# Kernel optimization log

Measured on AMD Instinct MI355X. Metric: run time of the kernel, lower is better.

The kernel has to match this reference:

```python
import jax, jax.numpy as jnp
from jax import lax
import numpy as np

# pywt sym4 analysis filters (pywt.Wavelet('sym4').dec_lo / .dec_hi)
DEC_LO = np.array([-0.07576571478927333, -0.02963552764599851, 0.49761866763201545,
                   0.8037387518059161, 0.29785779560527736, -0.09921954357684722,
                   -0.012603967262037833, 0.0322231006040427], dtype=np.float32)
DEC_HI = np.array([-0.0322231006040427, -0.012603967262037833, 0.09921954357684722,
                   0.29785779560527736, -0.8037387518059161, 0.49761866763201545,
                   0.02963552764599851, -0.07576571478927333], dtype=np.float32)
L = 8            # sym4 filter length
LEVEL = 4
THRESH = 10.0


def _conv1d(x, kernel, stride, pad):
    # x: (B, T), kernel: (L,) used in correlation sense by lax.conv
    y = lax.conv_general_dilated(x[:, None, :], kernel[None, None, :],
                                 window_strides=(stride,), padding=[pad],
                                 dimension_numbers=('NCH', 'OIH', 'NCH'))
    return y[:, 0, :]


def _dwt1(x, filt):
    # pywt single-level DWT, mode='symmetric':
    #   pad L-1 each side (half-sample symmetric), true convolution, take odd-index
    #   outputs of the 'valid' part -> length floor((N+L-1)/2)
    ext = jnp.pad(x, ((0, 0), (L - 1, L - 1)), mode='symmetric')[:, 1:]
    return _conv1d(ext, filt[::-1], 2, (0, 0))  # flip -> true convolution


def _idwt1(cA, cD, lo, hi):
    # pywt single-level IDWT: upsample by 2, full-convolve with rec filters, sum,
    # trim L-2 from the left, output length 2*n - L + 2.
    B, n = cA.shape
    upA = jnp.zeros((B, 2 * n), cA.dtype).at[:, ::2].set(cA)
    upD = jnp.zeros((B, 2 * n), cD.dtype).at[:, ::2].set(cD)
    # rec_lo = dec_lo[::-1]; full conv w/ rec_lo == correlation w/ dec_lo
    y = _conv1d(upA, lo, 1, (L - 1, L - 1)) + _conv1d(upD, hi, 1, (L - 1, L - 1))
    return y[:, L - 2: L - 2 + 2 * n - L + 2]


def _wavelet_denoise(x):
    lo = jnp.asarray(DEC_LO)
    hi = jnp.asarray(DEC_HI)
    a = x
    details = []
    for _ in range(LEVEL):
        details.append(_dwt1(a, hi))
        a = _dwt1(a, lo)
    # hard threshold: KEEP coefficients with |c| <= threshold, zero the rest
    details = [jnp.where(jnp.abs(d) <= THRESH, d, jnp.zeros_like(d)) for d in details]
    rec = a
    for d in reversed(details):
        if rec.shape[1] > d.shape[1]:     # pywt waverec a[:-1] trim
            rec = rec[:, :d.shape[1]]
        rec = _idwt1(rec, d, lo, hi)
    return rec


def setup_inputs() -> dict:
    key = jax.random.key(0)
    k1, k2 = jax.random.split(key)
    x = jax.random.normal(k1, (100000, 512), dtype=jnp.float32) * 20.0
    edge_index = jax.random.randint(k2, (2, 100000), 0, 100000, dtype=jnp.int64)
    return {"x": x, "edge_index": edge_index, "num_nodes": 100000}


def reference(x, edge_index, num_nodes):
    # edge_index / num_nodes are unused by the original forward
    return _wavelet_denoise(x)
```

## Files before the change

kernel.cpp:

```cpp
#include <hip/hip_runtime.h>
#include <cstddef>

typedef float f2 __attribute__((ext_vector_type(2)));
typedef float f4 __attribute__((ext_vector_type(4)));
typedef _Float16 h2 __attribute__((ext_vector_type(2)));
typedef _Float16 h8 __attribute__((ext_vector_type(8)));

#define THRESH_V 10.0f
#define WPB 2
#define SLICE_F2 930

static __device__ __forceinline__ void wave_sync() {
  asm volatile("s_waitcnt lgkmcnt(0)" ::: "memory");
}

#define L0f (-0.07576571478927333f)
#define L1f (-0.02963552764599851f)
#define L2f ( 0.49761866763201545f)
#define L3f ( 0.8037387518059161f)
#define L4f ( 0.29785779560527736f)
#define L5f (-0.09921954357684722f)
#define L6f (-0.012603967262037833f)
#define L7f ( 0.0322231006040427f)
#define H0f (-0.0322231006040427f)
#define H1f (-0.012603967262037833f)
#define H2f ( 0.09921954357684722f)
#define H3f ( 0.29785779560527736f)
#define H4f (-0.8037387518059161f)
#define H5f ( 0.49761866763201545f)
#define H6f ( 0.02963552764599851f)
#define H7f (-0.07576571478927333f)

static __device__ __forceinline__ f2 lo2(f4 w) { return __builtin_shufflevector(w, w, 0, 1); }
static __device__ __forceinline__ f2 hi2(f4 w) { return __builtin_shufflevector(w, w, 2, 3); }
static __device__ __forceinline__ float thr(float x) {
  return (fabsf(x) <= THRESH_V) ? x : 0.f;
}

template <int N, int B, bool MARGINS, bool D16>
static __device__ __forceinline__ void fwd_stage(const f2* __restrict__ in,
                                                 f2* __restrict__ ca,
                                                 void* __restrict__ cdv, int lane) {
#pragma clang fp contract(off)
  constexpr int M = (N + 7) >> 1;
  f2* const cdf = (f2*)cdv;
  h2* const cdh = (h2*)cdv;
  const int i0 = B * lane;
  if (i0 < M) {
    f2 w[2 * B + 6];
    const f4* p = (const f4*)(in + 2 * i0 - 6);
#pragma unroll
    for (int k = 0; k < B + 3; ++k) {
      const f4 t = p[k];
      w[2 * k] = lo2(t);
      w[2 * k + 1] = hi2(t);
    }
    f2 sA[B], sD[B];
#pragma unroll
    for (int j = 0; j < B; ++j) {
      const f2 v0 = w[2*j+0], v1 = w[2*j+1], v2 = w[2*j+2], v3 = w[2*j+3];
      const f2 v4 = w[2*j+4], v5 = w[2*j+5], v6 = w[2*j+6], v7 = w[2*j+7];
      f2 sLo = ((v0 * L7f + v1 * L6f) + (v2 * L5f + v3 * L4f)) +
               ((v4 * L3f + v5 * L2f) + (v6 * L1f + v7 * L0f));
      f2 sHi = ((v0 * H7f + v1 * H6f) + (v2 * H5f + v3 * H4f)) +
               ((v4 * H3f + v5 * H2f) + (v6 * H1f + v7 * H0f));
      sA[j] = sLo;
      f2 d; d.x = thr(sHi.x); d.y = thr(sHi.y);
      sD[j] = d;
      if constexpr (MARGINS) {
        const int i = i0 + j;
        if (i < 6)                 ca[-1 - i]        = sLo;
        if (i >= M - 7 && i < M)   ca[2 * M - 1 - i] = sLo;
      }
    }
    if (i0 + B <= M) {
      if constexpr (B == 4) {
        f4 c0; c0.x=sA[0].x; c0.y=sA[0].y; c0.z=sA[1].x; c0.w=sA[1].y;
        f4 c1; c1.x=sA[2].x; c1.y=sA[2].y; c1.z=sA[3].x; c1.w=sA[3].y;
        *(f4*)(ca + i0)     = c0;
        *(f4*)(ca + i0 + 2) = c1;
        if constexpr (D16) {
          h8 hv;
          hv[0]=(_Float16)sD[0].x; hv[1]=(_Float16)sD[0].y;
          hv[2]=(_Float16)sD[1].x; hv[3]=(_Float16)sD[1].y;
          hv[4]=(_Float16)sD[2].x; hv[5]=(_Float16)sD[2].y;
          hv[6]=(_Float16)sD[3].x; hv[7]=(_Float16)sD[3].y;
          *(h8*)(cdh + i0) = hv;
        } else {
          f4 d0; d0.x=sD[0].x; d0.y=sD[0].y; d0.z=sD[1].x; d0.w=sD[1].y;
          f4 d1; d1.x=sD[2].x; d1.y=sD[2].y; d1.z=sD[3].x; d1.w=sD[3].y;
          *(f4*)(cdf + i0)     = d0;
          *(f4*)(cdf + i0 + 2) = d1;
        }
      } else if constexpr (B == 2) {
        f4 c0; c0.x=sA[0].x; c0.y=sA[0].y; c0.z=sA[1].x; c0.w=sA[1].y;
        *(f4*)(ca + i0) = c0;
        if constexpr (D16) {
          h2 r0; r0.x=(_Float16)sD[0].x; r0.y=(_Float16)sD[0].y;
          h2 r1; r1.x=(_Float16)sD[1].x; r1.y=(_Float16)sD[1].y;
          cdh[i0] = r0; cdh[i0 + 1] = r1;
        } else {
          f4 d0; d0.x=sD[0].x; d0.y=sD[0].y; d0.z=sD[1].x; d0.w=sD[1].y;
          *(f4*)(cdf + i0) = d0;
        }
      } else {
#pragma unroll
        for (int j = 0; j < B; ++j) {
          ca[i0 + j] = sA[j];
          if constexpr (D16) {
            h2 r; r.x=(_Float16)sD[j].x; r.y=(_Float16)sD[j].y;
            cdh[i0 + j] = r;
          } else cdf[i0 + j] = sD[j];
        }
      }
    } else {
#pragma unroll
      for (int j = 0; j < B; ++j) {
        const int i = i0 + j;
        if (i < M) {
          ca[i] = sA[j];
          if constexpr (D16) {
            h2 r; r.x=(_Float16)sD[j].x; r.y=(_Float16)sD[j].y;
            cdh[i] = r;
          } else cdf[i] = sD[j];
        }
      }
    }
  }
  if constexpr (64 * B < M) {
    const int it = 64 * B + lane;
    if (it < M) {
      f2 w2[8];
      const f4* p2 = (const f4*)(in + 2 * it - 6);
#pragma unroll
      for (int k = 0; k < 4; ++k) { const f4 t = p2[k]; w2[2*k]=lo2(t); w2[2*k+1]=hi2(t); }
      const f2 v0=w2[0],v1=w2[1],v2=w2[2],v3=w2[3],v4=w2[4],v5=w2[5],v6=w2[6],v7=w2[7];
      f2 sLo = ((v0 * L7f + v1 * L6f) + (v2 * L5f + v3 * L4f)) +
               ((v4 * L3f + v5 * L2f) + (v6 * L1f + v7 * L0f));
      f2 sHi = ((v0 * H7f + v1 * H6f) + (v2 * H5f + v3 * H4f)) +
               ((v4 * H3f + v5 * H2f) + (v6 * H1f + v7 * H0f));
      ca[it] = sLo;
      if constexpr (MARGINS) {
        if (it >= M - 7) ca[2 * M - 1 - it] = sLo;
      }
      f2 d; d.x = thr(sHi.x); d.y = thr(sHi.y);
      if constexpr (D16) {
        h2 r; r.x=(_Float16)d.x; r.y=(_Float16)d.y;
        cdh[it] = r;
      } else cdf[it] = d;
    }
  }
}

template <int OUT, int B, bool D16, bool GOUT>
static __device__ __forceinline__ void inv_stage(const f2* __restrict__ ca,
                                                 const void* __restrict__ cdv,
                                                 f2* __restrict__ dst,
                                                 float* __restrict__ gA,
                                                 float* __restrict__ gB,
                                                 bool hasB, int lane) {
#pragma clang fp contract(fast)
  constexpr int P = (OUT + 1) >> 1;
  const f2* const cf = (const f2*)cdv;
  const h2* const ch = (const h2*)cdv;
  const int t0 = B * lane;
  if (t0 < P) {
    f2 a[B + 3], e[B + 3];
    if constexpr (B == 1) {
#pragma unroll
      for (int k = 0; k < 4; ++k) {
        a[k] = ca[t0 + k];
        if constexpr (D16) { const h2 hx = ch[t0+k]; e[k].x=(float)hx.x; e[k].y=(float)hx.y; }
        else e[k] = cf[t0 + k];
      }
    } else {
      constexpr int NR = (B + 4) / 2;
      const f4* pa = (const f4*)(ca + t0);
#pragma unroll
      for (int k = 0; k < NR; ++k) {
        const f4 t = pa[k];
        if (2 * k     < B + 3) a[2 * k]     = lo2(t);
        if (2 * k + 1 < B + 3) a[2 * k + 1] = hi2(t);
      }
      if constexpr (D16) {
        const f4* ph = (const f4*)(ch + t0);
        const f4 r0 = ph[0], r1 = ph[1];
        const float rr[8] = {r0.x, r0.y, r0.z, r0.w, r1.x, r1.y, r1.z, r1.w};
#pragma unroll
        for (int k = 0; k < B + 3; ++k) {
          const h2 hx = __builtin_bit_cast(h2, rr[k]);
          e[k].x = (float)hx.x; e[k].y = (float)hx.y;
        }
      } else {
        const f4* pe = (const f4*)(cf + t0);
#pragma unroll
        for (int k = 0; k < NR; ++k) {
          const f4 t = pe[k];
          if (2 * k     < B + 3) e[2 * k]     = lo2(t);
          if (2 * k + 1 < B + 3) e[2 * k + 1] = hi2(t);
        }
      }
    }
    f2 SE[B], SO[B];
#pragma unroll
    for (int j = 0; j < B; ++j) {
      const f2 a0=a[j], a1=a[j+1], a2=a[j+2], a3=a[j+3];
      const f2 e0=e[j], e1=e[j+1], e2=e[j+2], e3=e[j+3];
      SE[j] = a0*L1f + a1*L3f + a2*L5f + a3*L7f +
              e0*H1f + e1*H3f + e2*H5f + e3*H7f;
      SO[j] = a0*L0f + a1*L2f + a2*L4f + a3*L6f +
              e0*H0f + e1*H2f + e2*H4f + e3*H6f;
    }
    if constexpr (GOUT) {
      const int q0 = 2 * t0;
      *reinterpret_cast<float4*>(gA + q0)     = make_float4(SE[0].x, SO[0].x, SE[1].x, SO[1].x);
      *reinterpret_cast<float4*>(gA + q0 + 4) = make_float4(SE[2].x, SO[2].x, SE[3].x, SO[3].x);
      if (hasB) {
        *reinterpret_cast<float4*>(gB + q0)     = make_float4(SE[0].y, SO[0].y, SE[1].y, SO[1].y);
        *reinterpret_cast<float4*>(gB + q0 + 4) = make_float4(SE[2].y, SO[2].y, SE[3].y, SO[3].y);
      }
    } else {
      const bool full = (t0 + B <= P) && (2 * (t0 + B) <= OUT);
      if (full) {
#pragma unroll
        for (int j = 0; j < B; ++j) {
          f4 r; r.x=SE[j].x; r.y=SE[j].y; r.z=SO[j].x; r.w=SO[j].y;
          *(f4*)(dst + 2 * (t0 + j)) = r;
        }
      } else {
#pragma unroll
        for (int j = 0; j < B; ++j) {
          const int t = t0 + j;
          if (t < P) {
            const int q = 2 * t;
            dst[q] = SE[j];
            if (q + 1 < OUT) dst[q + 1] = SO[j];
          }
        }
      }
    }
  }
  if constexpr (64 * B < P) {
    const int tt = 64 * B + lane;
    if (tt < P) {
      const f2 a0=ca[tt], a1=ca[tt+1], a2=ca[tt+2], a3=ca[tt+3];
      f2 e0, e1, e2, e3;
      if constexpr (D16) {
        const h2 x0=ch[tt], x1=ch[tt+1], x2=ch[tt+2], x3=ch[tt+3];
        e0.x=(float)x0.x; e0.y=(float)x0.y; e1.x=(float)x1.x; e1.y=(float)x1.y;
        e2.x=(float)x2.x; e2.y=(float)x2.y; e3.x=(float)x3.x; e3.y=(float)x3.y;
      } else { e0=cf[tt]; e1=cf[tt+1]; e2=cf[tt+2]; e3=cf[tt+3]; }
      const f2 se = a0*L1f + a1*L3f + a2*L5f + a3*L7f +
                    e0*H1f + e1*H3f + e2*H5f + e3*H7f;
      const f2 so = a0*L0f + a1*L2f + a2*L4f + a3*L6f +
                    e0*H0f + e1*H2f + e2*H4f + e3*H6f;
      const int q = 2 * tt;
      dst[q] = se;
      if (q + 1 < OUT) dst[q + 1] = so;
    }
  }
}

__global__ __launch_bounds__(128, 5) void wavelet_denoise_kernel(
    const float* __restrict__ x, float* __restrict__ out, int nrows) {
  __shared__ __align__(16) f2 lds[WPB][SLICE_F2];
  const int wave = threadIdx.x >> 6;
  const int lane = threadIdx.x & 63;
  const int nPairs = (nrows + 1) >> 1;
  const int pairId = blockIdx.x * WPB + wave;
  if (pairId >= nPairs) return;

  const int rA = 2 * pairId;
  const bool hasB = (rA + 1) < nrows;
  const int rBc = hasB ? rA + 1 : rA;

  f2* Sp  = lds[wave];
  f2* sx  = Sp + 6;
  f2* ca2 = Sp + 6;    f2* d2 = Sp + 146;
  f2* ca3 = Sp + 286;  f2* d3 = Sp + 364;
  f2* ca4 = Sp + 436;  f2* d4 = Sp + 474;
  f2* rec133 = Sp + 0;
  f2* ca1 = Sp + 530;
  f2* rec70  = Sp + 524;
  f2* rec259 = Sp + 524;
  h2* d1  = (h2*)(Sp + 800);

  {
    const float4* sA4 = reinterpret_cast<const float4*>(x + (size_t)rA * 512);
    const float4* sB4 = reinterpret_cast<const float4*>(x + (size_t)rBc * 512);
#pragma unroll
    for (int kk = 0; kk < 2; ++kk) {
      const int c = lane + kk * 64;
      const float4 a = sA4[c];
      const float4 b = sB4[c];
      f4 u0; u0.x = a.x; u0.y = b.x; u0.z = a.y; u0.w = b.y;
      f4 u1; u1.x = a.z; u1.y = b.z; u1.z = a.w; u1.w = b.w;
      *reinterpret_cast<f4*>(sx + 4 * c)     = u0;
      *reinterpret_cast<f4*>(sx + 4 * c + 2) = u1;
      if (c == 0) {
        f4 m0; m0.x = a.y; m0.y = b.y; m0.z = a.x; m0.w = b.x;
        *reinterpret_cast<f4*>(sx - 2) = m0;
        f4 m1; m1.x = a.w; m1.y = b.w; m1.z = a.z; m1.w = b.z;
        *reinterpret_cast<f4*>(sx - 4) = m1;
      }
      if (c == 1) {
        f4 m; m.x = a.y; m.y = b.y; m.z = a.x; m.w = b.x;
        *reinterpret_cast<f4*>(sx - 6) = m;
      }
      if (c == 127) {
        f4 m0; m0.x = a.w; m0.y = b.w; m0.z = a.z; m0.w = b.z;
        *reinterpret_cast<f4*>(sx + 512) = m0;
        f4 m1; m1.x = a.y; m1.y = b.y; m1.z = a.x; m1.w = b.x;
        *reinterpret_cast<f4*>(sx + 514) = m1;
      }
      if (c == 126) {
        f4 m0; m0.x = a.w; m0.y = b.w; m0.z = a.z; m0.w = b.z;
        *reinterpret_cast<f4*>(sx + 516) = m0;
      }
    }
  }
  wave_sync();

  fwd_stage<512, 4, true,  true >(sx,  ca1, d1, lane); wave_sync();
  fwd_stage<259, 3, true,  false>(ca1, ca2, d2, lane); wave_sync();
  fwd_stage<133, 2, true,  false>(ca2, ca3, d3, lane); wave_sync();
  fwd_stage< 70, 1, false, false>(ca3, ca4, d4, lane); wave_sync();

  float* gA = out + (size_t)rA * 512;
  float* gB = out + (size_t)rBc * 512;
  inv_stage< 70, 1, false, false>(ca4,    d4, rec70,  nullptr, nullptr, false, lane);
  wave_sync();
  inv_stage<133, 2, false, false>(rec70,  d3, rec133, nullptr, nullptr, false, lane);
  wave_sync();
  inv_stage<259, 2, false, false>(rec133, d2, rec259, nullptr, nullptr, false, lane);
  wave_sync();
  inv_stage<512, 4, true,  true >(rec259, d1, nullptr, gA, gB, hasB, lane);
}

extern "C" void kernel_launch(void* const* d_in, const int* in_sizes, int n_in,
                              void* d_out, int out_size, void* d_ws, size_t ws_size,
                              hipStream_t stream) {
  const float* x = (const float*)d_in[0];
  float* out = (float*)d_out;
  const int nrows = in_sizes[0] / 512;
  const int nPairs = (nrows + 1) >> 1;
  const int grid = (nPairs + WPB - 1) / WPB;
  wavelet_denoise_kernel<<<dim3(grid), dim3(WPB * 64), 0, stream>>>(x, out, nrows);
}
```

Baseline: 339.1 us.

## Compute first DWT level from global loads and XOR-swizzle LDS layout

The first forward level now reads its input windows straight from global memory into registers, with symmetric padding handled in registers for edge lanes. This drops the initial staging of the interleaved input rows into LDS and one LDS round trip. All LDS buffers are renumbered as offsets into one slice and accessed through an XOR swizzle, which is meant to cut bank conflicts on the strided f4 accesses. In exchange, neighbouring lanes load overlapping global windows, so each input element is fetched about twice, and the swizzle adds integer work to every LDS address.

```diff
diff --git a/kernel.cpp b/kernel.cpp
--- a/kernel.cpp
+++ b/kernel.cpp
@@ -8,10 +8,26 @@
 
 #define THRESH_V 10.0f
 #define WPB 2
-#define SLICE_F2 930
+#define SLICE_F2 928
+
+#define CA2B 6
+#define D2B  146
+#define CA3B 286
+#define D3B  364
+#define CA4B 434
+#define D4B  472
+#define REC133B 0
+#define REC70B  510
+#define REC259B 510
+#define CA1B 516
+#define D1B  784
 
 static __device__ __forceinline__ void wave_sync() {
   asm volatile("s_waitcnt lgkmcnt(0)" ::: "memory");
+}
+
+static __device__ __forceinline__ int swz(int U) {
+  return U ^ (((U >> 4) & 7) << 1);
 }
 
 #define L0f (-0.07576571478927333f)
@@ -37,154 +53,91 @@
   return (fabsf(x) <= THRESH_V) ? x : 0.f;
 }
 
-template <int N, int B, bool MARGINS, bool D16>
-static __device__ __forceinline__ void fwd_stage(const f2* __restrict__ in,
-                                                 f2* __restrict__ ca,
-                                                 void* __restrict__ cdv, int lane) {
+static __device__ __forceinline__ void fwd_core(f2 v0, f2 v1, f2 v2, f2 v3,
+                                                f2 v4, f2 v5, f2 v6, f2 v7,
+                                                f2& sLo, f2& sHi) {
 #pragma clang fp contract(off)
+  sLo = ((v0 * L7f + v1 * L6f) + (v2 * L5f + v3 * L4f)) +
+        ((v4 * L3f + v5 * L2f) + (v6 * L1f + v7 * L0f));
+  sHi = ((v0 * H7f + v1 * H6f) + (v2 * H5f + v3 * H4f)) +
+        ((v4 * H3f + v5 * H2f) + (v6 * H1f + v7 * H0f));
+}
+
+template <int N, int B, bool MARGINS>
+static __device__ __forceinline__ void fwd_lds(f2* __restrict__ Sp, int INB,
+                                               int CAB, int DB, int lane) {
   constexpr int M = (N + 7) >> 1;
-  f2* const cdf = (f2*)cdv;
-  h2* const cdh = (h2*)cdv;
   const int i0 = B * lane;
   if (i0 < M) {
-    f2 w[2 * B + 6];
-    const f4* p = (const f4*)(in + 2 * i0 - 6);
+    f2 w[2 * (B + 3)];
+    const int u0 = INB + 2 * i0 - 6;
 #pragma unroll
     for (int k = 0; k < B + 3; ++k) {
-      const f4 t = p[k];
+      const f4 t = *(const f4*)(Sp + swz(u0 + 2 * k));
       w[2 * k] = lo2(t);
       w[2 * k + 1] = hi2(t);
     }
     f2 sA[B], sD[B];
 #pragma unroll
     for (int j = 0; j < B; ++j) {
-      const f2 v0 = w[2*j+0], v1 = w[2*j+1], v2 = w[2*j+2], v3 = w[2*j+3];
-      const f2 v4 = w[2*j+4], v5 = w[2*j+5], v6 = w[2*j+6], v7 = w[2*j+7];
-      f2 sLo = ((v0 * L7f + v1 * L6f) + (v2 * L5f + v3 * L4f)) +
-               ((v4 * L3f + v5 * L2f) + (v6 * L1f + v7 * L0f));
-      f2 sHi = ((v0 * H7f + v1 * H6f) + (v2 * H5f + v3 * H4f)) +
-               ((v4 * H3f + v5 * H2f) + (v6 * H1f + v7 * H0f));
-      sA[j] = sLo;
-      f2 d; d.x = thr(sHi.x); d.y = thr(sHi.y);
+      f2 lo, hi;
+      fwd_core(w[2*j+0], w[2*j+1], w[2*j+2], w[2*j+3],
+               w[2*j+4], w[2*j+5], w[2*j+6], w[2*j+7], lo, hi);
+      sA[j] = lo;
+      f2 d; d.x = thr(hi.x); d.y = thr(hi.y);
       sD[j] = d;
       if constexpr (MARGINS) {
         const int i = i0 + j;
-        if (i < 6)                 ca[-1 - i]        = sLo;
-        if (i >= M - 7 && i < M)   ca[2 * M - 1 - i] = sLo;
-      }
-    }
-    if (i0 + B <= M) {
-      if constexpr (B == 4) {
-        f4 c0; c0.x=sA[0].x; c0.y=sA[0].y; c0.z=sA[1].x; c0.w=sA[1].y;
-        f4 c1; c1.x=sA[2].x; c1.y=sA[2].y; c1.z=sA[3].x; c1.w=sA[3].y;
-        *(f4*)(ca + i0)     = c0;
-        *(f4*)(ca + i0 + 2) = c1;
-        if constexpr (D16) {
-          h8 hv;
-          hv[0]=(_Float16)sD[0].x; hv[1]=(_Float16)sD[0].y;
-          hv[2]=(_Float16)sD[1].x; hv[3]=(_Float16)sD[1].y;
-          hv[4]=(_Float16)sD[2].x; hv[5]=(_Float16)sD[2].y;
-          hv[6]=(_Float16)sD[3].x; hv[7]=(_Float16)sD[3].y;
-          *(h8*)(cdh + i0) = hv;
-        } else {
-          f4 d0; d0.x=sD[0].x; d0.y=sD[0].y; d0.z=sD[1].x; d0.w=sD[1].y;
-          f4 d1; d1.x=sD[2].x; d1.y=sD[2].y; d1.z=sD[3].x; d1.w=sD[3].y;
-          *(f4*)(cdf + i0)     = d0;
-          *(f4*)(cdf + i0 + 2) = d1;
-        }
-      } else if constexpr (B == 2) {
-        f4 c0; c0.x=sA[0].x; c0.y=sA[0].y; c0.z=sA[1].x; c0.w=sA[1].y;
-        *(f4*)(ca + i0) = c0;
-        if constexpr (D16) {
-          h2 r0; r0.x=(_Float16)sD[0].x; r0.y=(_Float16)sD[0].y;
-          h2 r1; r1.x=(_Float16)sD[1].x; r1.y=(_Float16)sD[1].y;
-          cdh[i0] = r0; cdh[i0 + 1] = r1;
-        } else {
-          f4 d0; d0.x=sD[0].x; d0.y=sD[0].y; d0.z=sD[1].x; d0.w=sD[1].y;
-          *(f4*)(cdf + i0) = d0;
-        }
-      } else {
-#pragma unroll
-        for (int j = 0; j < B; ++j) {
-          ca[i0 + j] = sA[j];
-          if constexpr (D16) {
-            h2 r; r.x=(_Float16)sD[j].x; r.y=(_Float16)sD[j].y;
-            cdh[i0 + j] = r;
-          } else cdf[i0 + j] = sD[j];
-        }
-      }
+        if (i < 6 && i < M)        Sp[swz(CAB - 1 - i)]         = lo;
+        if (i >= M - 7 && i < M)   Sp[swz(CAB + 2 * M - 1 - i)] = lo;
+      }
+    }
+    if constexpr (B == 2) {
+      f4 c; c.x = sA[0].x; c.y = sA[0].y; c.z = sA[1].x; c.w = sA[1].y;
+      *(f4*)(Sp + swz(CAB + i0)) = c;
+      f4 d; d.x = sD[0].x; d.y = sD[0].y; d.z = sD[1].x; d.w = sD[1].y;
+      *(f4*)(Sp + swz(DB + i0)) = d;
     } else {
 #pragma unroll
       for (int j = 0; j < B; ++j) {
         const int i = i0 + j;
         if (i < M) {
-          ca[i] = sA[j];
-          if constexpr (D16) {
-            h2 r; r.x=(_Float16)sD[j].x; r.y=(_Float16)sD[j].y;
-            cdh[i] = r;
-          } else cdf[i] = sD[j];
+          Sp[swz(CAB + i)] = sA[j];
+          Sp[swz(DB + i)]  = sD[j];
         }
       }
     }
   }
-  if constexpr (64 * B < M) {
-    const int it = 64 * B + lane;
-    if (it < M) {
-      f2 w2[8];
-      const f4* p2 = (const f4*)(in + 2 * it - 6);
-#pragma unroll
-      for (int k = 0; k < 4; ++k) { const f4 t = p2[k]; w2[2*k]=lo2(t); w2[2*k+1]=hi2(t); }
-      const f2 v0=w2[0],v1=w2[1],v2=w2[2],v3=w2[3],v4=w2[4],v5=w2[5],v6=w2[6],v7=w2[7];
-      f2 sLo = ((v0 * L7f + v1 * L6f) + (v2 * L5f + v3 * L4f)) +
-               ((v4 * L3f + v5 * L2f) + (v6 * L1f + v7 * L0f));
-      f2 sHi = ((v0 * H7f + v1 * H6f) + (v2 * H5f + v3 * H4f)) +
-               ((v4 * H3f + v5 * H2f) + (v6 * H1f + v7 * H0f));
-      ca[it] = sLo;
-      if constexpr (MARGINS) {
-        if (it >= M - 7) ca[2 * M - 1 - it] = sLo;
-      }
-      f2 d; d.x = thr(sHi.x); d.y = thr(sHi.y);
-      if constexpr (D16) {
-        h2 r; r.x=(_Float16)d.x; r.y=(_Float16)d.y;
-        cdh[it] = r;
-      } else cdf[it] = d;
-    }
-  }
 }
 
 template <int OUT, int B, bool D16, bool GOUT>
-static __device__ __forceinline__ void inv_stage(const f2* __restrict__ ca,
-                                                 const void* __restrict__ cdv,
-                                                 f2* __restrict__ dst,
-                                                 float* __restrict__ gA,
-                                                 float* __restrict__ gB,
-                                                 bool hasB, int lane) {
+static __device__ __forceinline__ void inv_lds(f2* __restrict__ Sp, int CAB,
+                                               int DB, int DSTB,
+                                               float* __restrict__ gA,
+                                               float* __restrict__ gB,
+                                               bool hasB, int lane) {
 #pragma clang fp contract(fast)
   constexpr int P = (OUT + 1) >> 1;
-  const f2* const cf = (const f2*)cdv;
-  const h2* const ch = (const h2*)cdv;
   const int t0 = B * lane;
   if (t0 < P) {
     f2 a[B + 3], e[B + 3];
     if constexpr (B == 1) {
 #pragma unroll
       for (int k = 0; k < 4; ++k) {
-        a[k] = ca[t0 + k];
-        if constexpr (D16) { const h2 hx = ch[t0+k]; e[k].x=(float)hx.x; e[k].y=(float)hx.y; }
-        else e[k] = cf[t0 + k];
+        a[k] = Sp[swz(CAB + t0 + k)];
+        e[k] = Sp[swz(DB + t0 + k)];
       }
     } else {
       constexpr int NR = (B + 4) / 2;
-      const f4* pa = (const f4*)(ca + t0);
 #pragma unroll
       for (int k = 0; k < NR; ++k) {
-        const f4 t = pa[k];
+        const f4 t = *(const f4*)(Sp + swz(CAB + t0 + 2 * k));
         if (2 * k     < B + 3) a[2 * k]     = lo2(t);
         if (2 * k + 1 < B + 3) a[2 * k + 1] = hi2(t);
       }
       if constexpr (D16) {
-        const f4* ph = (const f4*)(ch + t0);
-        const f4 r0 = ph[0], r1 = ph[1];
+        const f4 r0 = *(const f4*)(Sp + swz(DB + (t0 >> 1)));
+        const f4 r1 = *(const f4*)(Sp + swz(DB + (t0 >> 1) + 2));
         const float rr[8] = {r0.x, r0.y, r0.z, r0.w, r1.x, r1.y, r1.z, r1.w};
 #pragma unroll
         for (int k = 0; k < B + 3; ++k) {
@@ -192,10 +145,9 @@
           e[k].x = (float)hx.x; e[k].y = (float)hx.y;
         }
       } else {
-        const f4* pe = (const f4*)(cf + t0);
 #pragma unroll
         for (int k = 0; k < NR; ++k) {
-          const f4 t = pe[k];
+          const f4 t = *(const f4*)(Sp + swz(DB + t0 + 2 * k));
           if (2 * k     < B + 3) e[2 * k]     = lo2(t);
           if (2 * k + 1 < B + 3) e[2 * k + 1] = hi2(t);
         }
@@ -204,12 +156,10 @@
     f2 SE[B], SO[B];
 #pragma unroll
     for (int j = 0; j < B; ++j) {
-      const f2 a0=a[j], a1=a[j+1], a2=a[j+2], a3=a[j+3];
-      const f2 e0=e[j], e1=e[j+1], e2=e[j+2], e3=e[j+3];
-      SE[j] = a0*L1f + a1*L3f + a2*L5f + a3*L7f +
-              e0*H1f + e1*H3f + e2*H5f + e3*H7f;
-      SO[j] = a0*L0f + a1*L2f + a2*L4f + a3*L6f +
-              e0*H0f + e1*H2f + e2*H4f + e3*H6f;
+      SE[j] = a[j]*L1f + a[j+1]*L3f + a[j+2]*L5f + a[j+3]*L7f +
+              e[j]*H1f + e[j+1]*H3f + e[j+2]*H5f + e[j+3]*H7f;
+      SO[j] = a[j]*L0f + a[j+1]*L2f + a[j+2]*L4f + a[j+3]*L6f +
+              e[j]*H0f + e[j+1]*H2f + e[j+2]*H4f + e[j+3]*H6f;
     }
     if constexpr (GOUT) {
       const int q0 = 2 * t0;
@@ -224,8 +174,8 @@
       if (full) {
 #pragma unroll
         for (int j = 0; j < B; ++j) {
-          f4 r; r.x=SE[j].x; r.y=SE[j].y; r.z=SO[j].x; r.w=SO[j].y;
-          *(f4*)(dst + 2 * (t0 + j)) = r;
+          f4 r; r.x = SE[j].x; r.y = SE[j].y; r.z = SO[j].x; r.w = SO[j].y;
+          *(f4*)(Sp + swz(DSTB + 2 * (t0 + j))) = r;
         }
       } else {
 #pragma unroll
@@ -233,8 +183,8 @@
           const int t = t0 + j;
           if (t < P) {
             const int q = 2 * t;
-            dst[q] = SE[j];
-            if (q + 1 < OUT) dst[q + 1] = SO[j];
+            Sp[swz(DSTB + q)] = SE[j];
+            if (q + 1 < OUT) Sp[swz(DSTB + q + 1)] = SO[j];
           }
         }
       }
@@ -243,20 +193,17 @@
   if constexpr (64 * B < P) {
     const int tt = 64 * B + lane;
     if (tt < P) {
-      const f2 a0=ca[tt], a1=ca[tt+1], a2=ca[tt+2], a3=ca[tt+3];
-      f2 e0, e1, e2, e3;
-      if constexpr (D16) {
-        const h2 x0=ch[tt], x1=ch[tt+1], x2=ch[tt+2], x3=ch[tt+3];
-        e0.x=(float)x0.x; e0.y=(float)x0.y; e1.x=(float)x1.x; e1.y=(float)x1.y;
-        e2.x=(float)x2.x; e2.y=(float)x2.y; e3.x=(float)x3.x; e3.y=(float)x3.y;
-      } else { e0=cf[tt]; e1=cf[tt+1]; e2=cf[tt+2]; e3=cf[tt+3]; }
+      f2 a0 = Sp[swz(CAB + tt)],     a1 = Sp[swz(CAB + tt + 1)];
+      f2 a2 = Sp[swz(CAB + tt + 2)], a3 = Sp[swz(CAB + tt + 3)];
+      f2 e0 = Sp[swz(DB + tt)],      e1 = Sp[swz(DB + tt + 1)];
+      f2 e2 = Sp[swz(DB + tt + 2)],  e3 = Sp[swz(DB + tt + 3)];
       const f2 se = a0*L1f + a1*L3f + a2*L5f + a3*L7f +
                     e0*H1f + e1*H3f + e2*H5f + e3*H7f;
       const f2 so = a0*L0f + a1*L2f + a2*L4f + a3*L6f +
                     e0*H0f + e1*H2f + e2*H4f + e3*H6f;
       const int q = 2 * tt;
-      dst[q] = se;
-      if (q + 1 < OUT) dst[q + 1] = so;
+      Sp[swz(DSTB + q)] = se;
+      if (q + 1 < OUT) Sp[swz(DSTB + q + 1)] = so;
     }
   }
 }
@@ -273,68 +220,109 @@
   const int rA = 2 * pairId;
   const bool hasB = (rA + 1) < nrows;
   const int rBc = hasB ? rA + 1 : rA;
-
-  f2* Sp  = lds[wave];
-  f2* sx  = Sp + 6;
-  f2* ca2 = Sp + 6;    f2* d2 = Sp + 146;
-  f2* ca3 = Sp + 286;  f2* d3 = Sp + 364;
-  f2* ca4 = Sp + 436;  f2* d4 = Sp + 474;
-  f2* rec133 = Sp + 0;
-  f2* ca1 = Sp + 530;
-  f2* rec70  = Sp + 524;
-  f2* rec259 = Sp + 524;
-  h2* d1  = (h2*)(Sp + 800);
+  const float* __restrict__ xA = x + (size_t)rA * 512;
+  const float* __restrict__ xB = x + (size_t)rBc * 512;
+
+  f2* Sp = lds[wave];
 
   {
-    const float4* sA4 = reinterpret_cast<const float4*>(x + (size_t)rA * 512);
-    const float4* sB4 = reinterpret_cast<const float4*>(x + (size_t)rBc * 512);
-#pragma unroll
-    for (int kk = 0; kk < 2; ++kk) {
-      const int c = lane + kk * 64;
-      const float4 a = sA4[c];
-      const float4 b = sB4[c];
-      f4 u0; u0.x = a.x; u0.y = b.x; u0.z = a.y; u0.w = b.y;
-      f4 u1; u1.x = a.z; u1.y = b.z; u1.z = a.w; u1.w = b.w;
-      *reinterpret_cast<f4*>(sx + 4 * c)     = u0;
-      *reinterpret_cast<f4*>(sx + 4 * c + 2) = u1;
-      if (c == 0) {
-        f4 m0; m0.x = a.y; m0.y = b.y; m0.z = a.x; m0.w = b.x;
-        *reinterpret_cast<f4*>(sx - 2) = m0;
-        f4 m1; m1.x = a.w; m1.y = b.w; m1.z = a.z; m1.w = b.z;
-        *reinterpret_cast<f4*>(sx - 4) = m1;
-      }
-      if (c == 1) {
-        f4 m; m.x = a.y; m.y = b.y; m.z = a.x; m.w = b.x;
-        *reinterpret_cast<f4*>(sx - 6) = m;
-      }
-      if (c == 127) {
-        f4 m0; m0.x = a.w; m0.y = b.w; m0.z = a.z; m0.w = b.z;
-        *reinterpret_cast<f4*>(sx + 512) = m0;
-        f4 m1; m1.x = a.y; m1.y = b.y; m1.z = a.x; m1.w = b.x;
-        *reinterpret_cast<f4*>(sx + 514) = m1;
-      }
-      if (c == 126) {
-        f4 m0; m0.x = a.w; m0.y = b.w; m0.z = a.z; m0.w = b.z;
-        *reinterpret_cast<f4*>(sx + 516) = m0;
-      }
+    float aw[16], bw[16];
+    if (lane == 0) {
+      const float4 a0 = *(const float4*)(xA);
+      const float4 a1 = *(const float4*)(xA + 4);
+      const float4 b0 = *(const float4*)(xB);
+      const float4 b1 = *(const float4*)(xB + 4);
+      aw[8]=a0.x; aw[9]=a0.y; aw[10]=a0.z; aw[11]=a0.w;
+      aw[12]=a1.x; aw[13]=a1.y; aw[14]=a1.z; aw[15]=a1.w;
+      aw[7]=a0.x; aw[6]=a0.y; aw[5]=a0.z; aw[4]=a0.w;
+      aw[3]=a1.x; aw[2]=a1.y; aw[1]=0.f; aw[0]=0.f;
+      bw[8]=b0.x; bw[9]=b0.y; bw[10]=b0.z; bw[11]=b0.w;
+      bw[12]=b1.x; bw[13]=b1.y; bw[14]=b1.z; bw[15]=b1.w;
+      bw[7]=b0.x; bw[6]=b0.y; bw[5]=b0.z; bw[4]=b0.w;
+      bw[3]=b1.x; bw[2]=b1.y; bw[1]=0.f; bw[0]=0.f;
+    } else {
+      const float* pA = xA + 8 * lane - 8;
+      const float* pB = xB + 8 * lane - 8;
+      const float4 a0 = *(const float4*)(pA);
+      const float4 a1 = *(const float4*)(pA + 4);
+      const float4 a2 = *(const float4*)(pA + 8);
+      const float4 a3 = *(const float4*)(pA + 12);
+      const float4 b0 = *(const float4*)(pB);
+      const float4 b1 = *(const float4*)(pB + 4);
+      const float4 b2 = *(const float4*)(pB + 8);
+      const float4 b3 = *(const float4*)(pB + 12);
+      aw[0]=a0.x; aw[1]=a0.y; aw[2]=a0.z; aw[3]=a0.w;
+      aw[4]=a1.x; aw[5]=a1.y; aw[6]=a1.z; aw[7]=a1.w;
+      aw[8]=a2.x; aw[9]=a2.y; aw[10]=a2.z; aw[11]=a2.w;
+      aw[12]=a3.x; aw[13]=a3.y; aw[14]=a3.z; aw[15]=a3.w;
+      bw[0]=b0.x; bw[1]=b0.y; bw[2]=b0.z; bw[3]=b0.w;
+      bw[4]=b1.x; bw[5]=b1.y; bw[6]=b1.z; bw[7]=b1.w;
+      bw[8]=b2.x; bw[9]=b2.y; bw[10]=b2.z; bw[11]=b2.w;
+      bw[12]=b3.x; bw[13]=b3.y; bw[14]=b3.z; bw[15]=b3.w;
+    }
+    const int i0 = 4 * lane;
+    f2 sA[4], sD[4];
+#pragma unroll
+    for (int j = 0; j < 4; ++j) {
+      f2 v[8];
+#pragma unroll
+      for (int t = 0; t < 8; ++t) {
+        f2 vv; vv.x = aw[2*j + t + 2]; vv.y = bw[2*j + t + 2];
+        v[t] = vv;
+      }
+      f2 lo, hi;
+      fwd_core(v[0], v[1], v[2], v[3], v[4], v[5], v[6], v[7], lo, hi);
+      sA[j] = lo;
+      f2 d; d.x = thr(hi.x); d.y = thr(hi.y);
+      sD[j] = d;
+      const int i = i0 + j;
+      if (i < 6)    Sp[swz(CA1B - 1 - i)]   = lo;
+      if (i >= 252) Sp[swz(CA1B + 517 - i)] = lo;
+    }
+    f4 c0; c0.x=sA[0].x; c0.y=sA[0].y; c0.z=sA[1].x; c0.w=sA[1].y;
+    f4 c1; c1.x=sA[2].x; c1.y=sA[2].y; c1.z=sA[3].x; c1.w=sA[3].y;
+    *(f4*)(Sp + swz(CA1B + i0))     = c0;
+    *(f4*)(Sp + swz(CA1B + i0 + 2)) = c1;
+    h8 hv;
+    hv[0]=(_Float16)sD[0].x; hv[1]=(_Float16)sD[0].y;
+    hv[2]=(_Float16)sD[1].x; hv[3]=(_Float16)sD[1].y;
+    hv[4]=(_Float16)sD[2].x; hv[5]=(_Float16)sD[2].y;
+    hv[6]=(_Float16)sD[3].x; hv[7]=(_Float16)sD[3].y;
+    *(h8*)(Sp + swz(D1B + 2 * lane)) = hv;
+    if (lane < 3) {
+      const int i = 256 + lane;
+      f2 v[8];
+#pragma unroll
+      for (int t = 0; t < 8; ++t) {
+        const int k = 2 * i - 6 + t;
+        const int s = (k <= 511) ? k : 1023 - k;
+        f2 vv; vv.x = xA[s]; vv.y = xB[s];
+        v[t] = vv;
+      }
+      f2 lo, hi;
+      fwd_core(v[0], v[1], v[2], v[3], v[4], v[5], v[6], v[7], lo, hi);
+      Sp[swz(CA1B + i)] = lo;
+      Sp[swz(CA1B + 517 - i)] = lo;
+      const float dx = thr(hi.x), dy = thr(hi.y);
+      h2 r; r.x = (_Float16)dx; r.y = (_Float16)dy;
+      ((h2*)(Sp + swz(D1B + (i >> 1))))[i & 1] = r;
     }
   }
   wave_sync();
 
-  fwd_stage<512, 4, true,  true >(sx,  ca1, d1, lane); wave_sync();
-  fwd_stage<259, 3, true,  false>(ca1, ca2, d2, lane); wave_sync();
-  fwd_stage<133, 2, true,  false>(ca2, ca3, d3, lane); wave_sync();
-  fwd_stage< 70, 1, false, false>(ca3, ca4, d4, lane); wave_sync();
+  fwd_lds<259, 3, true >(Sp, CA1B, CA2B, D2B, lane); wave_sync();
+  fwd_lds<133, 2, true >(Sp, CA2B, CA3B, D3B, lane); wave_sync();
+  fwd_lds< 70, 1, false>(Sp, CA3B, CA4B, D4B, lane); wave_sync();
 
   float* gA = out + (size_t)rA * 512;
   float* gB = out + (size_t)rBc * 512;
-  inv_stage< 70, 1, false, false>(ca4,    d4, rec70,  nullptr, nullptr, false, lane);
+  inv_lds< 70, 1, false, false>(Sp, CA4B,   D4B, REC70B,  nullptr, nullptr, false, lane);
   wave_sync();
-  inv_stage<133, 2, false, false>(rec70,  d3, rec133, nullptr, nullptr, false, lane);
+  inv_lds<133, 2, false, false>(Sp, REC70B, D3B, REC133B, nullptr, nullptr, false, lane);
   wave_sync();
-  inv_stage<259, 2, false, false>(rec133, d2, rec259, nullptr, nullptr, false, lane);
+  inv_lds<259, 2, false, false>(Sp, REC133B, D2B, REC259B, nullptr, nullptr, false, lane);
   wave_sync();
-  inv_stage<512, 4, true,  true >(rec259, d1, nullptr, gA, gB, hasB, lane);
+  inv_lds<512, 4, true,  true >(Sp, REC259B, D1B, 0, gA, gB, hasB, lane);
 }
 
 extern "C" void kernel_launch(void* const* d_in, const int* in_sizes, int n_in,
```

After: 350.2 us. 3.3% more time.
